# Performance work log

Hardware: AMD Instinct MI355X
Metric: run time of the kernel (lower is better)

Reference implementation:

```python
import jax, jax.numpy as jnp
from jax import lax
import numpy as np


def setup_inputs() -> dict:
    key = jax.random.key(0)
    ks = jax.random.split(key, 9)
    B, T, H = 64, 4096, 128
    G = 4 * H
    s = 1.0 / np.sqrt(H)  # PyTorch LSTM default init scale
    return {
        "data": jax.random.normal(ks[0], (B, T, 1), dtype=jnp.float32),
        "h0": jax.random.normal(ks[1], (B, H), dtype=jnp.float32),
        "c0": jax.random.normal(ks[2], (B, H), dtype=jnp.float32),
        "W_ih": jax.random.uniform(ks[3], (G, 1), jnp.float32, -s, s),
        "W_hh": jax.random.uniform(ks[4], (G, H), jnp.float32, -s, s),
        "b_ih": jax.random.uniform(ks[5], (G,), jnp.float32, -s, s),
        "b_hh": jax.random.uniform(ks[6], (G,), jnp.float32, -s, s),
        "W_out": jax.random.uniform(ks[7], (1, H), jnp.float32, -s, s),
        "b_out": jax.random.uniform(ks[8], (1,), jnp.float32, -s, s),
    }


def reference(data, h0, c0, W_ih, W_hh, b_ih, b_hh, W_out, b_out):
    # Single-layer batch-first LSTM (PyTorch gate order i,f,g,o), then Linear on last step.
    H = h0.shape[-1]
    # Precompute input projections for all timesteps: [B, T, 4H] -> time-major [T, B, 4H]
    x_proj = jnp.einsum("bti,gi->btg", data, W_ih) + b_ih + b_hh
    x_proj = jnp.swapaxes(x_proj, 0, 1)

    def step(carry, xg):
        h, c = carry
        gates = xg + h @ W_hh.T  # [B, 4H]
        i = jax.nn.sigmoid(gates[:, 0 * H:1 * H])
        f = jax.nn.sigmoid(gates[:, 1 * H:2 * H])
        g = jnp.tanh(gates[:, 2 * H:3 * H])
        o = jax.nn.sigmoid(gates[:, 3 * H:4 * H])
        c = f * c + i * g
        h = o * jnp.tanh(c)
        return (h, c), None

    (hT, _), _ = lax.scan(step, (h0, c0), x_proj)
    # out[:, -1, :] of the LSTM is hT; final linear projection -> [B, 1]
    return hT @ W_out.T + b_out
```

## Files before the change

kernel.cpp:

```cpp
#include <hip/hip_runtime.h>
#include <math.h>

constexpr int Hdim = 128;
constexpr int TMAX = 4096;
constexpr int REPH = 136;

typedef _Float16 v2h __attribute__((ext_vector_type(2)));

template <int CTRL>
__device__ __forceinline__ float dppf(float v) {
  return __int_as_float(
      __builtin_amdgcn_update_dpp(0, __float_as_int(v), CTRL, 0xF, 0xF, true));
}

#if __has_builtin(__builtin_amdgcn_exp2f)
__device__ __forceinline__ float exp2_fast(float x) {
  return __builtin_amdgcn_exp2f(x);
}
#else
__device__ __forceinline__ float exp2_fast(float x) {
  return __expf(x * 0.6931471805599453f);
}
#endif

__global__ __launch_bounds__(512) void lstm_persist(
    const float* __restrict__ data, const float* __restrict__ h0,
    const float* __restrict__ c0, const float* __restrict__ W_ih,
    const float* __restrict__ W_hh, const float* __restrict__ b_ih,
    const float* __restrict__ b_hh, const float* __restrict__ W_out,
    const float* __restrict__ b_out, float* __restrict__ out, int T) {
  __shared__ __align__(16) float xs[TMAX];
  __shared__ __align__(16) _Float16 hrep[2][4 * REPH];

  const int b = blockIdx.x;
  const int tid = threadIdx.x;
  const int q = tid & 3;
  const int e = tid >> 2;

  {
    const float4* src = (const float4*)(data + (size_t)b * T);
    float4* dst = (float4*)xs;
    for (int i = tid; i < T / 4; i += 512) dst[i] = src[i];
  }

  constexpr float L2E = 1.44269504088896f;

  v2h w[4][16];
#pragma unroll
  for (int r = 0; r < 4; ++r) {
    const float Mr = (r == 2) ? 2.0f * L2E : -L2E;
    const float* wr = W_hh + (size_t)(e + 128 * r) * Hdim + 32 * q;
#pragma unroll
    for (int j = 0; j < 8; ++j) {
      float4 v = ((const float4*)wr)[j];
      w[r][2 * j + 0] = v2h{(_Float16)(Mr * v.x), (_Float16)(Mr * v.y)};
      w[r][2 * j + 1] = v2h{(_Float16)(Mr * v.z), (_Float16)(Mr * v.w)};
    }
  }

  const int row = e + 128 * q;
  const float MkL = (q == 2) ? 2.0f * L2E : -L2E;
  const float wihL = MkL * W_ih[row];
  const float bsL = MkL * (b_ih[row] + b_hh[row]);
  const float As = (q == 2) ? -2.0f : 1.0f;
  const float Bs = (q == 2) ? 1.0f : 0.0f;
  const bool qb0 = (q & 1) != 0;
  const bool qb1 = (q & 2) != 0;

  float c = c0[(size_t)b * Hdim + e];
  if (q == 0) {
    const _Float16 hh = (_Float16)h0[(size_t)b * Hdim + e];
    hrep[0][0 * REPH + e] = hh;
    hrep[0][1 * REPH + e] = hh;
    hrep[0][2 * REPH + e] = hh;
    hrep[0][3 * REPH + e] = hh;
  }
  __syncthreads();

  for (int t0 = 0; t0 < T; t0 += 4) {
    const float4 xv = *(const float4*)&xs[t0];
    const float xts[4] = {xv.x, xv.y, xv.z, xv.w};
#pragma unroll
    for (int u = 0; u < 4; ++u) {
      const int t = t0 + u;
      const v2h* hp = (const v2h*)(&hrep[t & 1][q * REPH + 32 * q]);
      v2h h2[16];
#pragma unroll
      for (int j = 0; j < 16; ++j) h2[j] = hp[j];

      float a0 = 0.f, a1 = 0.f, a2 = 0.f, a3 = 0.f;
#pragma unroll
      for (int j = 0; j < 16; ++j) {
        a0 = __builtin_amdgcn_fdot2(w[0][j], h2[j], a0, false);
        a1 = __builtin_amdgcn_fdot2(w[1][j], h2[j], a1, false);
        a2 = __builtin_amdgcn_fdot2(w[2][j], h2[j], a2, false);
        a3 = __builtin_amdgcn_fdot2(w[3][j], h2[j], a3, false);
      }

      float x01 = qb0 ? a1 : a0;
      float y01 = qb0 ? a0 : a1;
      x01 += dppf<0xB1>(y01);
      float x23 = qb0 ? a3 : a2;
      float y23 = qb0 ? a2 : a3;
      x23 += dppf<0xB1>(y23);
      float z = qb1 ? x23 : x01;
      float zz = qb1 ? x01 : x23;
      z += dppf<0x4E>(zz);

      const float pre = fmaf(xts[u], wihL, bsL) + z;
      const float y =
          fmaf(As, __builtin_amdgcn_rcpf(1.0f + exp2_fast(pre)), Bs);

      const float yi = dppf<0x00>(y);
      const float yf = dppf<0x55>(y);
      const float yg = dppf<0xAA>(y);
      const float yo = dppf<0xFF>(y);

      c = fmaf(yf, c, yi * yg);
      const float th = fmaf(
          -2.0f, __builtin_amdgcn_rcpf(1.0f + exp2_fast(c * (2.0f * L2E))),
          1.0f);
      const float h = yo * th;

      hrep[(t + 1) & 1][q * REPH + e] = (_Float16)h;
      __syncthreads();
    }
  }

  if (tid < 64) {
    const _Float16* hf = &hrep[T & 1][0];
    float sum =
        (float)hf[tid] * W_out[tid] + (float)hf[tid + 64] * W_out[tid + 64];
#pragma unroll
    for (int off = 32; off > 0; off >>= 1) sum += __shfl_down(sum, off, 64);
    if (tid == 0) out[b] = sum + b_out[0];
  }
}

extern "C" void kernel_launch(void* const* d_in, const int* in_sizes, int n_in,
                              void* d_out, int out_size, void* d_ws,
                              size_t ws_size, hipStream_t stream) {
  const float* data = (const float*)d_in[0];
  const float* h0 = (const float*)d_in[1];
  const float* c0 = (const float*)d_in[2];
  const float* W_ih = (const float*)d_in[3];
  const float* W_hh = (const float*)d_in[4];
  const float* b_ih = (const float*)d_in[5];
  const float* b_hh = (const float*)d_in[6];
  const float* W_out = (const float*)d_in[7];
  const float* b_out = (const float*)d_in[8];
  float* out = (float*)d_out;

  const int B = in_sizes[1] / Hdim;
  const int T = in_sizes[0] / B;

  lstm_persist<<<B, 512, 0, stream>>>(data, h0, c0, W_ih, W_hh, b_ih, b_hh,
                                      W_out, b_out, out, T);
}
```

Baseline: 1.938 ms.

## Compute recurrent matvec with MFMA and stage gate preactivations through LDS

```diff
diff --git a/kernel.cpp b/kernel.cpp
--- a/kernel.cpp
+++ b/kernel.cpp
@@ -3,9 +3,9 @@
 
 constexpr int Hdim = 128;
 constexpr int TMAX = 4096;
-constexpr int REPH = 136;
 
-typedef _Float16 v2h __attribute__((ext_vector_type(2)));
+typedef _Float16 v8h __attribute__((ext_vector_type(8)));
+typedef float v4f __attribute__((ext_vector_type(4)));
 
 template <int CTRL>
 __device__ __forceinline__ float dppf(float v) {
@@ -23,17 +23,22 @@
 }
 #endif
 
-__global__ __launch_bounds__(512) void lstm_persist(
+__global__ __launch_bounds__(512) void lstm_mfma(
     const float* __restrict__ data, const float* __restrict__ h0,
     const float* __restrict__ c0, const float* __restrict__ W_ih,
     const float* __restrict__ W_hh, const float* __restrict__ b_ih,
     const float* __restrict__ b_hh, const float* __restrict__ W_out,
     const float* __restrict__ b_out, float* __restrict__ out, int T) {
   __shared__ __align__(16) float xs[TMAX];
-  __shared__ __align__(16) _Float16 hrep[2][4 * REPH];
+  __shared__ __align__(16) _Float16 hbuf[2][Hdim];
+  __shared__ __align__(16) float pre[4 * 136];
 
   const int b = blockIdx.x;
   const int tid = threadIdx.x;
+  const int lane = tid & 63;
+  const int wv = tid >> 6;
+  const int p = lane >> 4;
+  const int m = lane & 15;
   const int q = tid & 3;
   const int e = tid >> 2;
 
@@ -45,90 +50,85 @@
 
   constexpr float L2E = 1.44269504088896f;
 
-  v2h w[4][16];
+  v8h a[4][4];
 #pragma unroll
-  for (int r = 0; r < 4; ++r) {
-    const float Mr = (r == 2) ? 2.0f * L2E : -L2E;
-    const float* wr = W_hh + (size_t)(e + 128 * r) * Hdim + 32 * q;
+  for (int i = 0; i < 4; ++i) {
+    const int row = 16 * (4 * wv + i) + m;
+    const float Mr = ((row >> 7) == 2) ? 2.0f * L2E : -L2E;
+    const float* wr = W_hh + (size_t)row * Hdim + 8 * p;
 #pragma unroll
-    for (int j = 0; j < 8; ++j) {
-      float4 v = ((const float4*)wr)[j];
-      w[r][2 * j + 0] = v2h{(_Float16)(Mr * v.x), (_Float16)(Mr * v.y)};
-      w[r][2 * j + 1] = v2h{(_Float16)(Mr * v.z), (_Float16)(Mr * v.w)};
+    for (int c = 0; c < 4; ++c) {
+      float4 v0 = ((const float4*)(wr + 32 * c))[0];
+      float4 v1 = ((const float4*)(wr + 32 * c))[1];
+      a[i][c] = v8h{(_Float16)(Mr * v0.x), (_Float16)(Mr * v0.y),
+                    (_Float16)(Mr * v0.z), (_Float16)(Mr * v0.w),
+                    (_Float16)(Mr * v1.x), (_Float16)(Mr * v1.y),
+                    (_Float16)(Mr * v1.z), (_Float16)(Mr * v1.w)};
     }
   }
 
-  const int row = e + 128 * q;
+  const int rowt = e + 128 * q;
   const float MkL = (q == 2) ? 2.0f * L2E : -L2E;
-  const float wihL = MkL * W_ih[row];
-  const float bsL = MkL * (b_ih[row] + b_hh[row]);
+  const float wihL = MkL * W_ih[rowt];
+  const float bsL = MkL * (b_ih[rowt] + b_hh[rowt]);
   const float As = (q == 2) ? -2.0f : 1.0f;
   const float Bs = (q == 2) ? 1.0f : 0.0f;
-  const bool qb0 = (q & 1) != 0;
-  const bool qb1 = (q & 2) != 0;
 
-  float c = c0[(size_t)b * Hdim + e];
-  if (q == 0) {
-    const _Float16 hh = (_Float16)h0[(size_t)b * Hdim + e];
-    hrep[0][0 * REPH + e] = hh;
-    hrep[0][1 * REPH + e] = hh;
-    hrep[0][2 * REPH + e] = hh;
-    hrep[0][3 * REPH + e] = hh;
-  }
+  float cst = c0[(size_t)b * Hdim + e];
+  if (q == 0) hbuf[0][e] = (_Float16)h0[(size_t)b * Hdim + e];
   __syncthreads();
 
-  for (int t0 = 0; t0 < T; t0 += 4) {
-    const float4 xv = *(const float4*)&xs[t0];
-    const float xts[4] = {xv.x, xv.y, xv.z, xv.w};
+#pragma unroll 2
+  for (int t = 0; t < T; ++t) {
+    const _Float16* hb = hbuf[t & 1];
+    v8h bq[4];
 #pragma unroll
-    for (int u = 0; u < 4; ++u) {
-      const int t = t0 + u;
-      const v2h* hp = (const v2h*)(&hrep[t & 1][q * REPH + 32 * q]);
-      v2h h2[16];
+    for (int c = 0; c < 4; ++c)
+      bq[c] = *(const v8h*)(hb + 32 * c + 8 * p);
+
+    v4f d[4];
 #pragma unroll
-      for (int j = 0; j < 16; ++j) h2[j] = hp[j];
+    for (int i = 0; i < 4; ++i) {
+      v4f acc = {0.f, 0.f, 0.f, 0.f};
+#pragma unroll
+      for (int c = 0; c < 4; ++c)
+        acc = __builtin_amdgcn_mfma_f32_16x16x32_f16(a[i][c], bq[c], acc,
+                                                     0, 0, 0);
+      d[i] = acc;
+    }
 
-      float a0 = 0.f, a1 = 0.f, a2 = 0.f, a3 = 0.f;
+    if (m == 0) {
 #pragma unroll
-      for (int j = 0; j < 16; ++j) {
-        a0 = __builtin_amdgcn_fdot2(w[0][j], h2[j], a0, false);
-        a1 = __builtin_amdgcn_fdot2(w[1][j], h2[j], a1, false);
-        a2 = __builtin_amdgcn_fdot2(w[2][j], h2[j], a2, false);
-        a3 = __builtin_amdgcn_fdot2(w[3][j], h2[j], a3, false);
+      for (int i = 0; i < 4; ++i) {
+        const int rowbase = 16 * (4 * wv + i);
+        const int addr = 136 * (rowbase >> 7) + (rowbase & 127) + 4 * p;
+        *(float4*)&pre[addr] = float4{d[i].x, d[i].y, d[i].z, d[i].w};
       }
+    }
+    const float xt = xs[t];
+    __syncthreads();
 
-      float x01 = qb0 ? a1 : a0;
-      float y01 = qb0 ? a0 : a1;
-      x01 += dppf<0xB1>(y01);
-      float x23 = qb0 ? a3 : a2;
-      float y23 = qb0 ? a2 : a3;
-      x23 += dppf<0xB1>(y23);
-      float z = qb1 ? x23 : x01;
-      float zz = qb1 ? x01 : x23;
-      z += dppf<0x4E>(zz);
+    const float z = pre[136 * q + e];
+    const float pg = fmaf(xt, wihL, bsL) + z;
+    const float y = fmaf(As, __builtin_amdgcn_rcpf(1.0f + exp2_fast(pg)), Bs);
 
-      const float pre = fmaf(xts[u], wihL, bsL) + z;
-      const float y =
-          fmaf(As, __builtin_amdgcn_rcpf(1.0f + exp2_fast(pre)), Bs);
+    const float yi = dppf<0x00>(y);
+    const float yf = dppf<0x55>(y);
+    const float yg = dppf<0xAA>(y);
+    const float yo = dppf<0xFF>(y);
 
-      const float yi = dppf<0x00>(y);
-      const float yf = dppf<0x55>(y);
-      const float yg = dppf<0xAA>(y);
-      const float yo = dppf<0xFF>(y);
+    cst = fmaf(yf, cst, yi * yg);
+    const float th = fmaf(
+        -2.0f, __builtin_amdgcn_rcpf(1.0f + exp2_fast(cst * (2.0f * L2E))),
+        1.0f);
+    const float h = yo * th;
 
-      c = fmaf(yf, c, yi * yg);
-      const float th = fmaf(
-          -2.0f, __builtin_amdgcn_rcpf(1.0f + exp2_fast(c * (2.0f * L2E))),
-          1.0f);
-      const float h = yo * th;
-
-      hrep[(t + 1) & 1][q * REPH + e] = (_Float16)h;
-      __syncthreads();
-    }
+    if (q == 0) hbuf[(t + 1) & 1][e] = (_Float16)h;
+    __syncthreads();
   }
 
   if (tid < 64) {
-    const _Float16* hf = &hrep[T & 1][0];
+    const _Float16* hf = hbuf[T & 1];
     float sum =
         (float)hf[tid] * W_out[tid] + (float)hf[tid + 64] * W_out[tid + 64];
 #pragma unroll
@@ -154,6 +154,6 @@
   const int B = in_sizes[1] / Hdim;
   const int T = in_sizes[0] / B;
 
-  lstm_persist<<<B, 512, 0, stream>>>(data, h0, c0, W_ih, W_hh, b_ih, b_hh,
-                                      W_out, b_out, out, T);
+  lstm_mfma<<<B, 512, 0, stream>>>(data, h0, c0, W_ih, W_hh, b_ih, b_hh,
+                                   W_out, b_out, out, T);
 }
```

New measurement: 2.406 ms. +24.1%, slower.
